# Kernel tuning notes

Measured on AMD Instinct MI355X. Metric: run time of the kernel, lower is better.

Reference implementation:

```python
import jax, jax.numpy as jnp
import numpy as np

N = 100_000      # nodes
E = 1_600_000    # edges (avg degree 16)
D = 64           # node feature dim
C = 2            # num_classes
K = 2            # propagation hops


def setup_inputs() -> dict:
    key = jax.random.key(0)
    k1, k2, k3 = jax.random.split(key, 3)
    x = jax.random.normal(k1, (N, D), dtype=jnp.float32)
    edge_index = jax.random.randint(k2, (2, E), 0, N, dtype=jnp.int64)
    W = jax.random.normal(k3, (C, D), dtype=jnp.float32) * 0.1  # torch Linear weight [out,in]
    b = jnp.zeros((C,), dtype=jnp.float32)
    return {"x": x, "edge_index": edge_index, "W": W, "b": b}


def reference(x, edge_index, W, b):
    n = x.shape[0]
    self_loop = jnp.arange(n, dtype=edge_index.dtype)
    row = jnp.concatenate([edge_index[0], self_loop])  # source
    col = jnp.concatenate([edge_index[1], self_loop])  # target
    # GCN symmetric normalization with self-loops (PyG gcn_norm)
    deg = jax.ops.segment_sum(jnp.ones(col.shape, dtype=x.dtype), col, num_segments=n)
    dinv = jnp.where(deg > 0, jax.lax.rsqrt(deg), 0.0)
    norm = dinv[row] * dinv[col]                      # [E+N]
    # K-hop propagation: x <- A_hat x
    for _ in range(K):
        x = jax.ops.segment_sum(norm[:, None] * x[row], col, num_segments=n)
    logits = x @ W.T + b                               # [N, C]
    return jax.nn.log_softmax(logits, axis=1)
```

## Files before the change

kernel.cpp:

```cpp
#include <hip/hip_runtime.h>
#include <hip/hip_bf16.h>
#include <math.h>


#define NODES 100000
#define EDGES 1600000
#define DIM 64

#define PBITS 8
#define PSIZE 256
#define P_BUCKETS 391
#define CAP 8192

#define PART_BLOCKS 256
#define PART_PAIRS (EDGES / 2 / PART_BLOCKS)

#define PROJ_BLOCKS 782
#define NODES_PER_PROJ 128
#define K1_BLOCKS (PART_BLOCKS + PROJ_BLOCKS)

__global__ void zero_kernel(int* __restrict__ cursor) {
  int i = threadIdx.x;
  if (i < P_BUCKETS) cursor[i] = 0;
}

__global__ __launch_bounds__(256) void partproj_kernel(
    const void* __restrict__ ei, int* __restrict__ cursor,
    int* __restrict__ ecbuf, const float* __restrict__ x,
    const float* __restrict__ W, float2* __restrict__ u) {
  const int t = threadIdx.x;
  if (blockIdx.x < PART_BLOCKS) {
    __shared__ int shMode;
    __shared__ int lcnt[P_BUCKETS];
    __shared__ int lbase[P_BUCKETS];
    if (t < 64) {
      const int* p = (const int*)ei;
      unsigned long long ball = __ballot(p[2 * t + 1] == 0);
      if (t == 0) shMode = (ball == ~0ULL) ? 1 : 0;
    }
    for (int i = t; i < P_BUCKETS; i += 256) lcnt[i] = 0;
    __syncthreads();
    const int m = shMode;
    const int pbase = blockIdx.x * PART_PAIRS;

    if (m) {
      const longlong2* cp =
          (const longlong2*)((const long long*)ei + EDGES) + pbase;
      for (int i = t; i < PART_PAIRS; i += 256) {
        longlong2 v = cp[i];
        atomicAdd(&lcnt[((int)v.x) >> PBITS], 1);
        atomicAdd(&lcnt[((int)v.y) >> PBITS], 1);
      }
    } else {
      const int2* cp = (const int2*)((const int*)ei + EDGES) + pbase;
      for (int i = t; i < PART_PAIRS; i += 256) {
        int2 v = cp[i];
        atomicAdd(&lcnt[v.x >> PBITS], 1);
        atomicAdd(&lcnt[v.y >> PBITS], 1);
      }
    }
    __syncthreads();
    for (int i = t; i < P_BUCKETS; i += 256) {
      int c = lcnt[i];
      lbase[i] = c ? atomicAdd(&cursor[i], c) : 0;
      lcnt[i] = 0;
    }
    __syncthreads();

    if (m) {
      const longlong2* rp = (const longlong2*)ei + pbase;
      const longlong2* cp =
          (const longlong2*)((const long long*)ei + EDGES) + pbase;
      for (int i = t; i < PART_PAIRS; i += 256) {
        longlong2 rv = rp[i];
        longlong2 cv = cp[i];
        {
          int r = (int)rv.x, c = (int)cv.x, bk = c >> PBITS;
          int rel = lbase[bk] + atomicAdd(&lcnt[bk], 1);
          if (rel < CAP)
            __builtin_nontemporal_store((r << PBITS) | (c & (PSIZE - 1)),
                                        &ecbuf[bk * CAP + rel]);
        }
        {
          int r = (int)rv.y, c = (int)cv.y, bk = c >> PBITS;
          int rel = lbase[bk] + atomicAdd(&lcnt[bk], 1);
          if (rel < CAP)
            __builtin_nontemporal_store((r << PBITS) | (c & (PSIZE - 1)),
                                        &ecbuf[bk * CAP + rel]);
        }
      }
    } else {
      const int2* rp = (const int2*)ei + pbase;
      const int2* cp = (const int2*)((const int*)ei + EDGES) + pbase;
      for (int i = t; i < PART_PAIRS; i += 256) {
        int2 rv = rp[i];
        int2 cv = cp[i];
        {
          int bk = cv.x >> PBITS;
          int rel = lbase[bk] + atomicAdd(&lcnt[bk], 1);
          if (rel < CAP)
            __builtin_nontemporal_store((rv.x << PBITS) | (cv.x & (PSIZE - 1)),
                                        &ecbuf[bk * CAP + rel]);
        }
        {
          int bk = cv.y >> PBITS;
          int rel = lbase[bk] + atomicAdd(&lcnt[bk], 1);
          if (rel < CAP)
            __builtin_nontemporal_store((rv.y << PBITS) | (cv.y & (PSIZE - 1)),
                                        &ecbuf[bk * CAP + rel]);
        }
      }
    }
  } else {
    const int nbase = (blockIdx.x - PART_BLOCKS) * NODES_PER_PROJ;
    const int lane16 = t & 15;
    const int sub = t >> 4;
    const float4 w0 = *(const float4*)&W[lane16 * 4];
    const float4 w1 = *(const float4*)&W[DIM + lane16 * 4];
    for (int k = sub; k < NODES_PER_PROJ; k += 16) {
      const int node = nbase + k;
      if (node < NODES) {
        float4 xv = *(const float4*)&x[(size_t)node * DIM + lane16 * 4];
        float p0 = xv.x * w0.x + xv.y * w0.y + xv.z * w0.z + xv.w * w0.w;
        float p1 = xv.x * w1.x + xv.y * w1.y + xv.z * w1.z + xv.w * w1.w;
#pragma unroll
        for (int off = 8; off >= 1; off >>= 1) {
          p0 += __shfl_xor(p0, off, 16);
          p1 += __shfl_xor(p1, off, 16);
        }
        if (lane16 == 0) u[node] = make_float2(p0, p1);
      }
    }
  }
}

__global__ __launch_bounds__(1024) void deg_kernel(
    const int* __restrict__ cursor, const int* __restrict__ ecbuf,
    const float2* __restrict__ u, float2* __restrict__ v2,
    float* __restrict__ dv) {
  __shared__ int h[PSIZE];
  const int b = blockIdx.x;
  const int t = threadIdx.x;
  if (t < PSIZE) h[t] = 0;
  __syncthreads();
  const int cnt = min(cursor[b], CAP);
  const int4* ep4 = (const int4*)(ecbuf + b * CAP);
  for (int i = t; 4 * i < cnt; i += 1024) {
    int4 v = ep4[i];
    int base = 4 * i;
    if (base + 0 < cnt) atomicAdd(&h[v.x & (PSIZE - 1)], 1);
    if (base + 1 < cnt) atomicAdd(&h[v.y & (PSIZE - 1)], 1);
    if (base + 2 < cnt) atomicAdd(&h[v.z & (PSIZE - 1)], 1);
    if (base + 3 < cnt) atomicAdd(&h[v.w & (PSIZE - 1)], 1);
  }
  __syncthreads();
  if (t < PSIZE) {
    const int node = (b << PBITS) + t;
    if (node < NODES) {
      float d = rsqrtf((float)(h[t] + 1));
      float2 uu = u[node];
      dv[node] = d;
      v2[node] = make_float2(d * uu.x, d * uu.y);
    }
  }
}

__global__ __launch_bounds__(1024) void hop1_kernel(
    const int* __restrict__ cursor, const int* __restrict__ ecbuf,
    const float2* __restrict__ v2, const float* __restrict__ dv,
    float2* __restrict__ z) {
  __shared__ float ax[PSIZE];
  __shared__ float ay[PSIZE];
  const int b = blockIdx.x;
  const int t = threadIdx.x;
  if (t < PSIZE) {
    ax[t] = 0.f;
    ay[t] = 0.f;
  }
  __syncthreads();
  const int cnt = min(cursor[b], CAP);
  const int4* ep4 = (const int4*)(ecbuf + b * CAP);
  for (int i = t; 4 * i < cnt; i += 1024) {
    int4 v = ep4[i];
    int base = 4 * i;
#pragma unroll
    for (int k = 0; k < 4; k++) {
      int pk = (k == 0) ? v.x : (k == 1) ? v.y : (k == 2) ? v.z : v.w;
      if (base + k < cnt) {
        float2 s = v2[pk >> PBITS];
        int l = pk & (PSIZE - 1);
        atomicAdd(&ax[l], s.x);
        atomicAdd(&ay[l], s.y);
      }
    }
  }
  __syncthreads();
  if (t < PSIZE) {
    const int node = (b << PBITS) + t;
    if (node < NODES) {
      float d = dv[node];
      float sc = d * d;
      float2 vs = v2[node];
      z[node] = make_float2(sc * (ax[t] + vs.x), sc * (ay[t] + vs.y));
    }
  }
}

__global__ __launch_bounds__(1024) void hop2_kernel(
    const int* __restrict__ cursor, const int* __restrict__ ecbuf,
    const float2* __restrict__ z, const float* __restrict__ dv,
    const float* __restrict__ bias, float2* __restrict__ out) {
  __shared__ float ax[PSIZE];
  __shared__ float ay[PSIZE];
  const int b = blockIdx.x;
  const int t = threadIdx.x;
  if (t < PSIZE) {
    ax[t] = 0.f;
    ay[t] = 0.f;
  }
  __syncthreads();
  const int cnt = min(cursor[b], CAP);
  const int4* ep4 = (const int4*)(ecbuf + b * CAP);
  for (int i = t; 4 * i < cnt; i += 1024) {
    int4 v = ep4[i];
    int base = 4 * i;
#pragma unroll
    for (int k = 0; k < 4; k++) {
      int pk = (k == 0) ? v.x : (k == 1) ? v.y : (k == 2) ? v.z : v.w;
      if (base + k < cnt) {
        float2 zv = z[pk >> PBITS];
        int l = pk & (PSIZE - 1);
        atomicAdd(&ax[l], zv.x);
        atomicAdd(&ay[l], zv.y);
      }
    }
  }
  __syncthreads();
  if (t < PSIZE) {
    const int node = (b << PBITS) + t;
    if (node < NODES) {
      float d = dv[node];
      float2 zi = z[node];
      float l0 = d * (ax[t] + zi.x) + bias[0];
      float l1 = d * (ay[t] + zi.y) + bias[1];
      float m = fmaxf(l0, l1);
      float ls = m + logf(expf(l0 - m) + expf(l1 - m));
      out[node] = make_float2(l0 - ls, l1 - ls);
    }
  }
}

extern "C" void kernel_launch(void* const* d_in, const int* in_sizes, int n_in,
                              void* d_out, int out_size, void* d_ws,
                              size_t ws_size, hipStream_t stream) {
  const float* x = (const float*)d_in[0];
  const void* ei = d_in[1];
  const float* W = (const float*)d_in[2];
  const float* bias = (const float*)d_in[3];
  float2* out = (float2*)d_out;

  char* w = (char*)d_ws;
  size_t off = 0;
  auto alloc = [&](size_t bytes) -> char* {
    char* p = w + off;
    off += (bytes + 255) & ~(size_t)255;
    return p;
  };
  const int NPAD = P_BUCKETS << PBITS;
  int* cursor = (int*)alloc(P_BUCKETS * sizeof(int));
  int* ecbuf = (int*)alloc((size_t)P_BUCKETS * CAP * sizeof(int));
  float2* u = (float2*)alloc((size_t)NPAD * sizeof(float2));
  float2* v2 = (float2*)alloc((size_t)NPAD * sizeof(float2));
  float* dv = (float*)alloc((size_t)NPAD * sizeof(float));
  float2* z = (float2*)alloc((size_t)NPAD * sizeof(float2));
  (void)ws_size;

  zero_kernel<<<1, 512, 0, stream>>>(cursor);
  partproj_kernel<<<K1_BLOCKS, 256, 0, stream>>>(ei, cursor, ecbuf, x, W, u);
  deg_kernel<<<P_BUCKETS, 1024, 0, stream>>>(cursor, ecbuf, u, v2, dv);
  hop1_kernel<<<P_BUCKETS, 1024, 0, stream>>>(cursor, ecbuf, v2, dv, z);
  hop2_kernel<<<P_BUCKETS, 1024, 0, stream>>>(cursor, ecbuf, z, dv, bias, out);
}
```

Before: 174.1 us.

## Replace global bucket cursors with per-block local partitions and offset scan

Each partition block now writes its edges into its own contiguous chunk, sorted by destination bucket through a shared-memory prefix scan, and publishes per-bucket offsets. The zero kernel and the global atomic cursors go away. Consumer kernels now read, for each bucket, 256 scattered segments (two threads per source block) instead of one contiguous capped buffer. This removes the cross-block atomics, the CAP overflow limit and one launch, but it makes the edge reads in the three consumer kernels shorter, unvectorized and less coalesced, and the block size drops to 512.

New measurement: 151.1 us. 13.2% less time.

```diff
diff --git a/kernel.cpp b/kernel.cpp
--- a/kernel.cpp
+++ b/kernel.cpp
@@ -10,38 +10,36 @@
 #define PBITS 8
 #define PSIZE 256
 #define P_BUCKETS 391
-#define CAP 8192
 
 #define PART_BLOCKS 256
-#define PART_PAIRS (EDGES / 2 / PART_BLOCKS)
+#define ECHUNK (EDGES / PART_BLOCKS)
+#define PART_PAIRS (ECHUNK / 2)
+#define SCANW (P_BUCKETS + 1)
 
 #define PROJ_BLOCKS 782
 #define NODES_PER_PROJ 128
 #define K1_BLOCKS (PART_BLOCKS + PROJ_BLOCKS)
 
-__global__ void zero_kernel(int* __restrict__ cursor) {
-  int i = threadIdx.x;
-  if (i < P_BUCKETS) cursor[i] = 0;
-}
-
 __global__ __launch_bounds__(256) void partproj_kernel(
-    const void* __restrict__ ei, int* __restrict__ cursor,
-    int* __restrict__ ecbuf, const float* __restrict__ x,
+    const void* __restrict__ ei, int* __restrict__ bscan,
+    int* __restrict__ eloc, const float* __restrict__ x,
     const float* __restrict__ W, float2* __restrict__ u) {
   const int t = threadIdx.x;
   if (blockIdx.x < PART_BLOCKS) {
-    __shared__ int shMode;
+    __shared__ int sMode;
     __shared__ int lcnt[P_BUCKETS];
-    __shared__ int lbase[P_BUCKETS];
+    __shared__ int sA[512];
+    __shared__ int sB[512];
     if (t < 64) {
       const int* p = (const int*)ei;
       unsigned long long ball = __ballot(p[2 * t + 1] == 0);
-      if (t == 0) shMode = (ball == ~0ULL) ? 1 : 0;
+      if (t == 0) sMode = (ball == ~0ULL) ? 1 : 0;
     }
     for (int i = t; i < P_BUCKETS; i += 256) lcnt[i] = 0;
     __syncthreads();
-    const int m = shMode;
-    const int pbase = blockIdx.x * PART_PAIRS;
+    const int m = sMode;
+    const int blk = blockIdx.x;
+    const int pbase = blk * PART_PAIRS;
 
     if (m) {
       const longlong2* cp =
@@ -60,13 +58,25 @@
       }
     }
     __syncthreads();
-    for (int i = t; i < P_BUCKETS; i += 256) {
-      int c = lcnt[i];
-      lbase[i] = c ? atomicAdd(&cursor[i], c) : 0;
-      lcnt[i] = 0;
-    }
-    __syncthreads();
-
+
+    for (int i = t; i < 512; i += 256) sA[i] = (i < P_BUCKETS) ? lcnt[i] : 0;
+    __syncthreads();
+    int* srcb = sA;
+    int* dstb = sB;
+    for (int off = 1; off < 512; off <<= 1) {
+      for (int i = t; i < 512; i += 256)
+        dstb[i] = srcb[i] + ((i >= off) ? srcb[i - off] : 0);
+      __syncthreads();
+      int* tmp = srcb;
+      srcb = dstb;
+      dstb = tmp;
+    }
+    for (int i = t; i < SCANW; i += 256)
+      bscan[blk * SCANW + i] = i ? srcb[i - 1] : 0;
+    for (int i = t; i < P_BUCKETS; i += 256) lcnt[i] = 0;
+    __syncthreads();
+
+    int* myloc = eloc + blk * ECHUNK;
     if (m) {
       const longlong2* rp = (const longlong2*)ei + pbase;
       const longlong2* cp =
@@ -76,17 +86,13 @@
         longlong2 cv = cp[i];
         {
           int r = (int)rv.x, c = (int)cv.x, bk = c >> PBITS;
-          int rel = lbase[bk] + atomicAdd(&lcnt[bk], 1);
-          if (rel < CAP)
-            __builtin_nontemporal_store((r << PBITS) | (c & (PSIZE - 1)),
-                                        &ecbuf[bk * CAP + rel]);
+          int pos = (bk ? srcb[bk - 1] : 0) + atomicAdd(&lcnt[bk], 1);
+          myloc[pos] = (r << PBITS) | (c & (PSIZE - 1));
         }
         {
           int r = (int)rv.y, c = (int)cv.y, bk = c >> PBITS;
-          int rel = lbase[bk] + atomicAdd(&lcnt[bk], 1);
-          if (rel < CAP)
-            __builtin_nontemporal_store((r << PBITS) | (c & (PSIZE - 1)),
-                                        &ecbuf[bk * CAP + rel]);
+          int pos = (bk ? srcb[bk - 1] : 0) + atomicAdd(&lcnt[bk], 1);
+          myloc[pos] = (r << PBITS) | (c & (PSIZE - 1));
         }
       }
     } else {
@@ -97,17 +103,13 @@
         int2 cv = cp[i];
         {
           int bk = cv.x >> PBITS;
-          int rel = lbase[bk] + atomicAdd(&lcnt[bk], 1);
-          if (rel < CAP)
-            __builtin_nontemporal_store((rv.x << PBITS) | (cv.x & (PSIZE - 1)),
-                                        &ecbuf[bk * CAP + rel]);
+          int pos = (bk ? srcb[bk - 1] : 0) + atomicAdd(&lcnt[bk], 1);
+          myloc[pos] = (rv.x << PBITS) | (cv.x & (PSIZE - 1));
         }
         {
           int bk = cv.y >> PBITS;
-          int rel = lbase[bk] + atomicAdd(&lcnt[bk], 1);
-          if (rel < CAP)
-            __builtin_nontemporal_store((rv.y << PBITS) | (cv.y & (PSIZE - 1)),
-                                        &ecbuf[bk * CAP + rel]);
+          int pos = (bk ? srcb[bk - 1] : 0) + atomicAdd(&lcnt[bk], 1);
+          myloc[pos] = (rv.y << PBITS) | (cv.y & (PSIZE - 1));
         }
       }
     }
@@ -134,8 +136,8 @@
   }
 }
 
-__global__ __launch_bounds__(1024) void deg_kernel(
-    const int* __restrict__ cursor, const int* __restrict__ ecbuf,
+__global__ __launch_bounds__(512) void degv_kernel(
+    const int* __restrict__ bscan, const int* __restrict__ eloc,
     const float2* __restrict__ u, float2* __restrict__ v2,
     float* __restrict__ dv) {
   __shared__ int h[PSIZE];
@@ -143,16 +145,11 @@
   const int t = threadIdx.x;
   if (t < PSIZE) h[t] = 0;
   __syncthreads();
-  const int cnt = min(cursor[b], CAP);
-  const int4* ep4 = (const int4*)(ecbuf + b * CAP);
-  for (int i = t; 4 * i < cnt; i += 1024) {
-    int4 v = ep4[i];
-    int base = 4 * i;
-    if (base + 0 < cnt) atomicAdd(&h[v.x & (PSIZE - 1)], 1);
-    if (base + 1 < cnt) atomicAdd(&h[v.y & (PSIZE - 1)], 1);
-    if (base + 2 < cnt) atomicAdd(&h[v.z & (PSIZE - 1)], 1);
-    if (base + 3 < cnt) atomicAdd(&h[v.w & (PSIZE - 1)], 1);
-  }
+  const int s = t >> 1, j = t & 1;
+  const int s0 = bscan[s * SCANW + b];
+  const int s1 = bscan[s * SCANW + b + 1];
+  const int* ep = eloc + s * ECHUNK;
+  for (int e = s0 + j; e < s1; e += 2) atomicAdd(&h[ep[e] & (PSIZE - 1)], 1);
   __syncthreads();
   if (t < PSIZE) {
     const int node = (b << PBITS) + t;
@@ -165,8 +162,8 @@
   }
 }
 
-__global__ __launch_bounds__(1024) void hop1_kernel(
-    const int* __restrict__ cursor, const int* __restrict__ ecbuf,
+__global__ __launch_bounds__(512) void hop1_kernel(
+    const int* __restrict__ bscan, const int* __restrict__ eloc,
     const float2* __restrict__ v2, const float* __restrict__ dv,
     float2* __restrict__ z) {
   __shared__ float ax[PSIZE];
@@ -178,21 +175,16 @@
     ay[t] = 0.f;
   }
   __syncthreads();
-  const int cnt = min(cursor[b], CAP);
-  const int4* ep4 = (const int4*)(ecbuf + b * CAP);
-  for (int i = t; 4 * i < cnt; i += 1024) {
-    int4 v = ep4[i];
-    int base = 4 * i;
-#pragma unroll
-    for (int k = 0; k < 4; k++) {
-      int pk = (k == 0) ? v.x : (k == 1) ? v.y : (k == 2) ? v.z : v.w;
-      if (base + k < cnt) {
-        float2 s = v2[pk >> PBITS];
-        int l = pk & (PSIZE - 1);
-        atomicAdd(&ax[l], s.x);
-        atomicAdd(&ay[l], s.y);
-      }
-    }
+  const int s = t >> 1, j = t & 1;
+  const int s0 = bscan[s * SCANW + b];
+  const int s1 = bscan[s * SCANW + b + 1];
+  const int* ep = eloc + s * ECHUNK;
+  for (int e = s0 + j; e < s1; e += 2) {
+    int pk = ep[e];
+    float2 v = v2[pk >> PBITS];
+    int l = pk & (PSIZE - 1);
+    atomicAdd(&ax[l], v.x);
+    atomicAdd(&ay[l], v.y);
   }
   __syncthreads();
   if (t < PSIZE) {
@@ -206,8 +198,8 @@
   }
 }
 
-__global__ __launch_bounds__(1024) void hop2_kernel(
-    const int* __restrict__ cursor, const int* __restrict__ ecbuf,
+__global__ __launch_bounds__(512) void hop2_kernel(
+    const int* __restrict__ bscan, const int* __restrict__ eloc,
     const float2* __restrict__ z, const float* __restrict__ dv,
     const float* __restrict__ bias, float2* __restrict__ out) {
   __shared__ float ax[PSIZE];
@@ -219,21 +211,16 @@
     ay[t] = 0.f;
   }
   __syncthreads();
-  const int cnt = min(cursor[b], CAP);
-  const int4* ep4 = (const int4*)(ecbuf + b * CAP);
-  for (int i = t; 4 * i < cnt; i += 1024) {
-    int4 v = ep4[i];
-    int base = 4 * i;
-#pragma unroll
-    for (int k = 0; k < 4; k++) {
-      int pk = (k == 0) ? v.x : (k == 1) ? v.y : (k == 2) ? v.z : v.w;
-      if (base + k < cnt) {
-        float2 zv = z[pk >> PBITS];
-        int l = pk & (PSIZE - 1);
-        atomicAdd(&ax[l], zv.x);
-        atomicAdd(&ay[l], zv.y);
-      }
-    }
+  const int s = t >> 1, j = t & 1;
+  const int s0 = bscan[s * SCANW + b];
+  const int s1 = bscan[s * SCANW + b + 1];
+  const int* ep = eloc + s * ECHUNK;
+  for (int e = s0 + j; e < s1; e += 2) {
+    int pk = ep[e];
+    float2 zv = z[pk >> PBITS];
+    int l = pk & (PSIZE - 1);
+    atomicAdd(&ax[l], zv.x);
+    atomicAdd(&ay[l], zv.y);
   }
   __syncthreads();
   if (t < PSIZE) {
@@ -267,17 +254,16 @@
     return p;
   };
   const int NPAD = P_BUCKETS << PBITS;
-  int* cursor = (int*)alloc(P_BUCKETS * sizeof(int));
-  int* ecbuf = (int*)alloc((size_t)P_BUCKETS * CAP * sizeof(int));
+  int* bscan = (int*)alloc((size_t)PART_BLOCKS * SCANW * sizeof(int));
+  int* eloc = (int*)alloc((size_t)EDGES * sizeof(int));
   float2* u = (float2*)alloc((size_t)NPAD * sizeof(float2));
   float2* v2 = (float2*)alloc((size_t)NPAD * sizeof(float2));
   float* dv = (float*)alloc((size_t)NPAD * sizeof(float));
   float2* z = (float2*)alloc((size_t)NPAD * sizeof(float2));
   (void)ws_size;
 
-  zero_kernel<<<1, 512, 0, stream>>>(cursor);
-  partproj_kernel<<<K1_BLOCKS, 256, 0, stream>>>(ei, cursor, ecbuf, x, W, u);
-  deg_kernel<<<P_BUCKETS, 1024, 0, stream>>>(cursor, ecbuf, u, v2, dv);
-  hop1_kernel<<<P_BUCKETS, 1024, 0, stream>>>(cursor, ecbuf, v2, dv, z);
-  hop2_kernel<<<P_BUCKETS, 1024, 0, stream>>>(cursor, ecbuf, z, dv, bias, out);
-}
+  partproj_kernel<<<K1_BLOCKS, 256, 0, stream>>>(ei, bscan, eloc, x, W, u);
+  degv_kernel<<<P_BUCKETS, 512, 0, stream>>>(bscan, eloc, u, v2, dv);
+  hop1_kernel<<<P_BUCKETS, 512, 0, stream>>>(bscan, eloc, v2, dv, z);
+  hop2_kernel<<<P_BUCKETS, 512, 0, stream>>>(bscan, eloc, z, dv, bias, out);
+}
```
